# Optimization experiments

Measured on AMD Instinct MI355X. Metric: run time of the kernel, lower is better.

The kernel has to match this reference:

```python
import jax, jax.numpy as jnp
import numpy as np

K = 3          # number of nearest neighbors (pointops.interpolation uses k=3)
CHUNK = 4096   # fine-point chunk size for blocked kNN (bounds peak memory)
EPS = 1e-8     # inverse-distance epsilon, matches pointops interpolation


def _interpolate(xyz1, xyz2, feature2):
    """3-NN inverse-distance weighted interpolation from coarse (xyz2, feature2)
    onto fine points xyz1. Single batch (offsets cover all points)."""
    n1 = xyz1.shape[0]
    x2_sq = jnp.sum(xyz2 * xyz2, axis=-1)  # [N2]
    chunks = xyz1.reshape(n1 // CHUNK, CHUNK, 3)

    def body(q):  # q: [CHUNK, 3]
        q_sq = jnp.sum(q * q, axis=-1, keepdims=True)          # [CHUNK, 1]
        d2 = q_sq + x2_sq[None, :] - 2.0 * (q @ xyz2.T)        # [CHUNK, N2]
        neg_d2, idx = jax.lax.top_k(-d2, K)                    # 3 smallest
        dist = jnp.sqrt(jnp.maximum(-neg_d2, 1e-12))           # euclidean
        w = 1.0 / (dist + EPS)
        w = w / jnp.sum(w, axis=-1, keepdims=True)             # [CHUNK, K]
        return jnp.einsum('qk,qkc->qc', w, feature2[idx])      # [CHUNK, C]

    out = jax.lax.map(body, chunks)  # [n_chunks, CHUNK, C]
    return out.reshape(n1, -1)


def setup_inputs() -> dict:
    key = jax.random.key(0)
    k1, k2, k3, k4, k5, k6 = jax.random.split(key, 6)
    N1, N2, C, OUT = 32768, 8192, 256, 256
    xyz1 = jax.random.normal(k1, (N1, 3), dtype=jnp.float32)
    xyz2 = jax.random.normal(k2, (N2, 3), dtype=jnp.float32)
    feature1 = jax.random.normal(k3, (N1, C), dtype=jnp.float32)
    feature2 = jax.random.normal(k4, (N2, C), dtype=jnp.float32)
    offset1 = jnp.array([N1], dtype=jnp.int32)
    offset2 = jnp.array([N2], dtype=jnp.int32)
    W = jax.random.normal(k5, (OUT, C), dtype=jnp.float32) * (1.0 / np.sqrt(C))
    b = jax.random.normal(k6, (OUT,), dtype=jnp.float32) * 0.01
    return {"xyz1": xyz1, "xyz2": xyz2, "feature1": feature1,
            "feature2": feature2, "offset1": offset1, "offset2": offset2,
            "W": W, "b": b}


def reference(xyz1, xyz2, feature1, feature2, offset1, offset2, W, b):
    interp = _interpolate(xyz1, xyz2, feature2)  # [N1, C]
    return interp @ W.T + b                      # nn.Linear(in_coarse, out)
```

## Files before the change

kernel.cpp:

```cpp
#include <hip/hip_runtime.h>


#define FLT_BIG 3.402823466e+38f
#define CAP     16
#define MARGIN  3e-5f

__device__ __forceinline__ float rlf(float v, int l) {
    return __uint_as_float((unsigned)__builtin_amdgcn_readlane((int)__float_as_uint(v), l));
}

__global__ __launch_bounds__(256) void prep_kernel(const float* __restrict__ xyz2,
                                                   float4* __restrict__ pack, int N2) {
    int j = blockIdx.x * 256 + threadIdx.x;
    if (j < N2) {
        float x = xyz2[3 * j + 0];
        float y = xyz2[3 * j + 1];
        float z = xyz2[3 * j + 2];
        float4 p;
        p.x = x; p.y = y; p.z = z;
        p.w = 0.5f * (x * x + y * y + z * z);
        pack[j] = p;
    }
}

__global__ __launch_bounds__(256) void gemm_nt_f32(const float* __restrict__ A,
                                                   const float* __restrict__ B,
                                                   float* __restrict__ C,
                                                   int M, int N, int K) {
    __shared__ float As[64][68];
    __shared__ float Bs[64][68];

    const int t  = threadIdx.x;
    const int tx = t & 15;
    const int ty = t >> 4;
    const int bm = blockIdx.x * 64;
    const int bn = blockIdx.y * 64;

    float acc[4][4] = {{0.f}};

    for (int kt = 0; kt < K; kt += 64) {
#pragma unroll
        for (int rr = 0; rr < 4; ++rr) {
            int r = ty + 16 * rr;
            int c = tx * 4;
            float4 av = *(const float4*)(A + (size_t)(bm + r) * K + kt + c);
            As[c + 0][r] = av.x;
            As[c + 1][r] = av.y;
            As[c + 2][r] = av.z;
            As[c + 3][r] = av.w;
            float4 bv = *(const float4*)(B + (size_t)(bn + r) * K + kt + c);
            Bs[c + 0][r] = bv.x;
            Bs[c + 1][r] = bv.y;
            Bs[c + 2][r] = bv.z;
            Bs[c + 3][r] = bv.w;
        }
        __syncthreads();

#pragma unroll 8
        for (int k = 0; k < 64; ++k) {
            float4 a4 = *(const float4*)&As[k][ty * 4];
            float4 b4 = *(const float4*)&Bs[k][tx * 4];
            float a[4] = {a4.x, a4.y, a4.z, a4.w};
            float b[4] = {b4.x, b4.y, b4.z, b4.w};
#pragma unroll
            for (int i = 0; i < 4; ++i)
#pragma unroll
                for (int j = 0; j < 4; ++j)
                    acc[i][j] = fmaf(a[i], b[j], acc[i][j]);
        }
        __syncthreads();
    }

#pragma unroll
    for (int i = 0; i < 4; ++i) {
        float4 v;
        v.x = acc[i][0]; v.y = acc[i][1]; v.z = acc[i][2]; v.w = acc[i][3];
        *(float4*)(C + (size_t)(bm + ty * 4 + i) * N + bn + tx * 4) = v;
    }
}

#define TOP4V_INSERT(mv)                                           \
    do {                                                           \
        float _x  = (mv);                                          \
        float _n0 = fminf(b0, _x);  float _y0 = fmaxf(b0, _x); b0 = _n0; \
        float _n1 = fminf(b1, _y0); float _y1 = fmaxf(b1, _y0); b1 = _n1; \
        float _n2 = fminf(b2, _y1); float _y2 = fmaxf(b2, _y1); b2 = _n2; \
        b3 = fminf(b3, _y2);                                       \
    } while (0)

#define TOP3JD_INSERT(dd, j)                                       \
    do {                                                           \
        bool lt2 = ((dd) < d2v) || ((dd) == d2v && (j) < j2);      \
        if (lt2) {                                                 \
            bool lt1 = ((dd) < d1) || ((dd) == d1 && (j) < j1);    \
            if (lt1) {                                             \
                d2v = d1; j2 = j1;                                 \
                bool lt0 = ((dd) < d0) || ((dd) == d0 && (j) < j0);\
                if (lt0) { d1 = d0; j1 = j0; d0 = (dd); j0 = (j); }\
                else     { d1 = (dd); j1 = (j); }                  \
            } else { d2v = (dd); j2 = (j); }                       \
        }                                                          \
    } while (0)

#define DECLS(s) float px##s, py##s, pz##s, pw##s;
#define LOADS(s) { float4 _p = pack[base + ((s) << 6) + lane]; \
                   px##s = _p.x; py##s = _p.y; pz##s = _p.z; pw##s = _p.w; }
#define SAMPW(s) samp[wave][((s) << 6) + lane] = make_float4(px##s, py##s, pz##s, pw##s);
#define SLOTF(s)                                                               \
    {                                                                          \
        float acc = fmaf(qxx, px##s, fmaf(qyy, py##s, fmaf(qzz, pz##s, tq))); \
        unsigned long long mk = __ballot(acc >= pw##s);                        \
        while (mk) {                                                           \
            int l = __builtin_ctzll(mk);                                       \
            mk &= mk - 1;                                                      \
            if (is0 && cnt < CAP)                                              \
                myring[cnt] = (unsigned short)(base + ((s) << 6) + l);         \
            ++cnt;                                                             \
        }                                                                      \
    }
#define X16(M) M(0) M(1) M(2) M(3) M(4) M(5) M(6) M(7) \
               M(8) M(9) M(10) M(11) M(12) M(13) M(14) M(15)
#define X4(M)  M(0) M(1) M(2) M(3)

__global__ __launch_bounds__(512, 4) void knn_gather(const float* __restrict__ xyz1,
                                                     const float4* __restrict__ pack,
                                                     const float4* __restrict__ G4,
                                                     const float4* __restrict__ bias4,
                                                     float4* __restrict__ out4,
                                                     int N2) {
    __shared__ float4         samp[8][256];
    __shared__ float          mdl[64][25];
    __shared__ float          mdl4[64][33];
    __shared__ int            mil[64][25];
    __shared__ float          thr[64];
    __shared__ unsigned short ring[64][8 * CAP + 1];
    __shared__ unsigned short cnts[64][8];
    __shared__ float          swgt[64][3];
    __shared__ int            sidx[64][3];

    const int tid  = threadIdx.x;
    const int wave = __builtin_amdgcn_readfirstlane(tid >> 6);
    const int lane = tid & 63;
    const int fine = blockIdx.x * 64 + lane;

    const float qx = xyz1[3 * fine + 0];
    const float qy = xyz1[3 * fine + 1];
    const float qz = xyz1[3 * fine + 2];

    const int chunk = N2 >> 3;
    const int base  = wave * chunk;

    X16(DECLS)
    X16(LOADS)
    X4(SAMPW)
    __syncthreads();

    {
        float b0 = FLT_BIG, b1 = FLT_BIG, b2 = FLT_BIG, b3 = FLT_BIG;
        const float4* sp = samp[wave];
#pragma unroll 2
        for (int k = 0; k < 256; k += 4) {
            float4 p0 = sp[k + 0];
            float4 p1 = sp[k + 1];
            float4 p2 = sp[k + 2];
            float4 p3 = sp[k + 3];
            float m0 = p0.w - fmaf(qx, p0.x, fmaf(qy, p0.y, qz * p0.z));
            float m1 = p1.w - fmaf(qx, p1.x, fmaf(qy, p1.y, qz * p1.z));
            float m2 = p2.w - fmaf(qx, p2.x, fmaf(qy, p2.y, qz * p2.z));
            float m3 = p3.w - fmaf(qx, p3.x, fmaf(qy, p3.y, qz * p3.z));
            float mm = fminf(fminf(m0, m1), fminf(m2, m3));
            TOP4V_INSERT(mm);
        }
        mdl4[lane][wave * 4 + 0] = b0;
        mdl4[lane][wave * 4 + 1] = b1;
        mdl4[lane][wave * 4 + 2] = b2;
        mdl4[lane][wave * 4 + 3] = b3;
    }
    __syncthreads();

    if (tid < 64) {
        float b0 = FLT_BIG, b1 = FLT_BIG, b2 = FLT_BIG, b3 = FLT_BIG;
#pragma unroll
        for (int w = 0; w < 8; ++w)
#pragma unroll
            for (int k = 0; k < 4; ++k)
                TOP4V_INSERT(mdl4[tid][w * 4 + k]);
        thr[tid] = b3 + MARGIN;
    }
    __syncthreads();

    {
        const float qt_own = thr[lane];
        const bool  is0    = (lane == 0);
#pragma unroll 1
        for (int q = 0; q < 64; ++q) {
            float qxx = rlf(qx, q);
            float qyy = rlf(qy, q);
            float qzz = rlf(qz, q);
            float tq  = rlf(qt_own, q);
            int cnt = 0;
            unsigned short* myring = &ring[q][wave * CAP];
            X16(SLOTF)
            if (is0) cnts[q][wave] = (unsigned short)(cnt < CAP ? cnt : CAP);
        }
    }
    __syncthreads();

    {
        const int q  = tid >> 3;
        const int w  = tid & 7;
        const int fq = blockIdx.x * 64 + q;
        const float sqx = xyz1[3 * fq + 0];
        const float sqy = xyz1[3 * fq + 1];
        const float sqz = xyz1[3 * fq + 2];
        const float qsq = __fadd_rn(__fadd_rn(__fmul_rn(sqx, sqx), __fmul_rn(sqy, sqy)),
                                    __fmul_rn(sqz, sqz));
        float d0 = FLT_BIG, d1 = FLT_BIG, d2v = FLT_BIG;
        int   j0 = 0x7fffffff, j1 = 0x7fffffff, j2 = 0x7fffffff;
        const int n = (int)cnts[q][w];
        for (int e = 0; e < n; ++e) {
            const int j = ring[q][w * CAP + e];
            float4 p = pack[j];
            float x2s = __fadd_rn(__fadd_rn(__fmul_rn(p.x, p.x), __fmul_rn(p.y, p.y)),
                                  __fmul_rn(p.z, p.z));
            float dot = __fmaf_rn(sqz, p.z, __fmaf_rn(sqy, p.y, __fmul_rn(sqx, p.x)));
            float dd = __fsub_rn(__fadd_rn(qsq, x2s), __fmul_rn(2.0f, dot));
            TOP3JD_INSERT(dd, j);
        }
        mdl[q][w * 3 + 0] = d0;  mdl[q][w * 3 + 1] = d1;  mdl[q][w * 3 + 2] = d2v;
        mil[q][w * 3 + 0] = j0;  mil[q][w * 3 + 1] = j1;  mil[q][w * 3 + 2] = j2;
    }
    __syncthreads();

    if (tid < 64) {
        float d0 = FLT_BIG, d1 = FLT_BIG, d2v = FLT_BIG;
        int   j0 = 0x7fffffff, j1 = 0x7fffffff, j2 = 0x7fffffff;
#pragma unroll
        for (int w = 0; w < 8; ++w)
#pragma unroll
            for (int k = 0; k < 3; ++k) {
                float dd = mdl[tid][w * 3 + k];
                int   j  = mil[tid][w * 3 + k];
                TOP3JD_INSERT(dd, j);
            }
        float w0 = 1.0f / (__fadd_rn(sqrtf(fmaxf(d0,  1e-12f)), 1e-8f));
        float w1 = 1.0f / (__fadd_rn(sqrtf(fmaxf(d1,  1e-12f)), 1e-8f));
        float w2 = 1.0f / (__fadd_rn(sqrtf(fmaxf(d2v, 1e-12f)), 1e-8f));
        float wsum = __fadd_rn(__fadd_rn(w0, w1), w2);
        swgt[tid][0] = w0 / wsum; sidx[tid][0] = j0;
        swgt[tid][1] = w1 / wsum; sidx[tid][1] = j1;
        swgt[tid][2] = w2 / wsum; sidx[tid][2] = j2;
    }
    __syncthreads();

    const float4 bb = bias4[lane];
#pragma unroll
    for (int p = 0; p < 8; ++p) {
        int fl = wave * 8 + p;
        float w0 = swgt[fl][0];
        float w1 = swgt[fl][1];
        float w2 = swgt[fl][2];
        int j0 = sidx[fl][0];
        int j1 = sidx[fl][1];
        int j2 = sidx[fl][2];
        float4 g0 = G4[(size_t)j0 * 64 + lane];
        float4 g1 = G4[(size_t)j1 * 64 + lane];
        float4 g2 = G4[(size_t)j2 * 64 + lane];
        float4 o;
        o.x = fmaf(w0, g0.x, fmaf(w1, g1.x, fmaf(w2, g2.x, bb.x)));
        o.y = fmaf(w0, g0.y, fmaf(w1, g1.y, fmaf(w2, g2.y, bb.y)));
        o.z = fmaf(w0, g0.z, fmaf(w1, g1.z, fmaf(w2, g2.z, bb.z)));
        o.w = fmaf(w0, g0.w, fmaf(w1, g1.w, fmaf(w2, g2.w, bb.w)));
        out4[(size_t)(blockIdx.x * 64 + fl) * 64 + lane] = o;
    }
}

extern "C" void kernel_launch(void* const* d_in, const int* in_sizes, int n_in,
                              void* d_out, int out_size, void* d_ws, size_t ws_size,
                              hipStream_t stream) {
    const float* xyz1 = (const float*)d_in[0];
    const float* xyz2 = (const float*)d_in[1];
    const float* f2   = (const float*)d_in[3];
    const float* W    = (const float*)d_in[6];
    const float* bias = (const float*)d_in[7];

    const int N1  = in_sizes[0] / 3;
    const int N2  = in_sizes[1] / 3;
    const int C   = in_sizes[3] / N2;
    const int OUT = in_sizes[7];

    float*  G    = (float*)d_ws;
    float4* pack = (float4*)((char*)d_ws + (size_t)N2 * OUT * 4);

    prep_kernel<<<(N2 + 255) / 256, 256, 0, stream>>>(xyz2, pack, N2);

    dim3 ggrid(N2 / 64, OUT / 64);
    gemm_nt_f32<<<ggrid, 256, 0, stream>>>(f2, W, G, N2, OUT, C);

    knn_gather<<<N1 / 64, 512, 0, stream>>>(xyz1, pack, (const float4*)G,
                                            (const float4*)bias, (float4*)d_out, N2);
}
```

Before: 117.7 us.

## Use lane broadcasts instead of LDS samples and full candidate scan over all coarse points

Phase 1 drops the shared-memory sample buffer and its barrier: each wave keeps its 256 sample points in registers and broadcasts them with readlane. Phase 2 no longer holds only 1024 coarse points per wave. It now loops over four chunks of 256 points loaded from global memory, accumulating per-query counts through readlane/select. The point is to cut register pressure and LDS traffic so the occupancy hint in launch_bounds can be dropped. When the candidate ring overflows, the refinement step falls back to a brute-force scan of the wave's 1024 points for correctness. The cost is more scalar readlane work, a hardcoded 1024-point-per-wave split that assumes N2=8192, and a possibly expensive fallback path.

```diff
diff --git a/kernel.cpp b/kernel.cpp
--- a/kernel.cpp
+++ b/kernel.cpp
@@ -2,7 +2,8 @@
 
 
 #define FLT_BIG 3.402823466e+38f
-#define CAP     16
+#define CAP     14
+#define RROW    (8 * CAP + 1)
 #define MARGIN  3e-5f
 
 __device__ __forceinline__ float rlf(float v, int l) {
@@ -102,39 +103,53 @@
         }                                                          \
     } while (0)
 
-#define DECLS(s) float px##s, py##s, pz##s, pw##s;
-#define LOADS(s) { float4 _p = pack[base + ((s) << 6) + lane]; \
-                   px##s = _p.x; py##s = _p.y; pz##s = _p.z; pw##s = _p.w; }
-#define SAMPW(s) samp[wave][((s) << 6) + lane] = make_float4(px##s, py##s, pz##s, pw##s);
-#define SLOTF(s)                                                               \
+#define REF_D2(p)                                                              \
+    __fsub_rn(__fadd_rn(qsq, __fadd_rn(__fadd_rn(__fmul_rn((p).x, (p).x),      \
+                                                 __fmul_rn((p).y, (p).y)),     \
+                                       __fmul_rn((p).z, (p).z))),              \
+              __fmul_rn(2.0f, __fmaf_rn(sqz, (p).z,                            \
+                                __fmaf_rn(sqy, (p).y, __fmul_rn(sqx, (p).x)))))
+
+#define PH1_CHUNK(ch)                                                          \
+    for (int j = 0; j < 64; j += 4) {                                          \
+        float mm = FLT_BIG;                                                    \
+        _Pragma("unroll")                                                      \
+        for (int u = 0; u < 4; ++u) {                                          \
+            float sx = rlf(ch.x, j + u);                                       \
+            float sy = rlf(ch.y, j + u);                                       \
+            float sz = rlf(ch.z, j + u);                                       \
+            float sw = rlf(ch.w, j + u);                                       \
+            mm = fminf(mm, sw - fmaf(qx, sx, fmaf(qy, sy, qz * sz)));          \
+        }                                                                      \
+        TOP4V_INSERT(mm);                                                      \
+    }
+
+#define PH2_CHUNK(ch, cidx)                                                    \
     {                                                                          \
-        float acc = fmaf(qxx, px##s, fmaf(qyy, py##s, fmaf(qzz, pz##s, tq))); \
-        unsigned long long mk = __ballot(acc >= pw##s);                        \
+        float acc = fmaf(qxx, ch.x, fmaf(qyy, ch.y, fmaf(qzz, ch.z, tq)));     \
+        unsigned long long mk = __ballot(acc >= ch.w);                         \
         while (mk) {                                                           \
             int l = __builtin_ctzll(mk);                                       \
             mk &= mk - 1;                                                      \
-            if (is0 && cnt < CAP)                                              \
-                myring[cnt] = (unsigned short)(base + ((s) << 6) + l);         \
-            ++cnt;                                                             \
+            if (lane == 0 && cs < CAP)                                         \
+                ring[q][wave * CAP + cs] =                                     \
+                    (unsigned short)(obase + (cidx) * 64 + l);                 \
+            ++cs;                                                              \
         }                                                                      \
     }
-#define X16(M) M(0) M(1) M(2) M(3) M(4) M(5) M(6) M(7) \
-               M(8) M(9) M(10) M(11) M(12) M(13) M(14) M(15)
-#define X4(M)  M(0) M(1) M(2) M(3)
-
-__global__ __launch_bounds__(512, 4) void knn_gather(const float* __restrict__ xyz1,
-                                                     const float4* __restrict__ pack,
-                                                     const float4* __restrict__ G4,
-                                                     const float4* __restrict__ bias4,
-                                                     float4* __restrict__ out4,
-                                                     int N2) {
-    __shared__ float4         samp[8][256];
+
+__global__ __launch_bounds__(512) void knn_gather(const float* __restrict__ xyz1,
+                                                  const float4* __restrict__ pack,
+                                                  const float4* __restrict__ G4,
+                                                  const float4* __restrict__ bias4,
+                                                  float4* __restrict__ out4,
+                                                  int N2) {
+    __shared__ float          mdl4[64][33];
+    __shared__ float          thr[64];
+    __shared__ unsigned short ring[64][RROW];
+    __shared__ unsigned char  cnts[64][8];
     __shared__ float          mdl[64][25];
-    __shared__ float          mdl4[64][33];
     __shared__ int            mil[64][25];
-    __shared__ float          thr[64];
-    __shared__ unsigned short ring[64][8 * CAP + 1];
-    __shared__ unsigned short cnts[64][8];
     __shared__ float          swgt[64][3];
     __shared__ int            sidx[64][3];
 
@@ -147,30 +162,18 @@
     const float qy = xyz1[3 * fine + 1];
     const float qz = xyz1[3 * fine + 2];
 
-    const int chunk = N2 >> 3;
-    const int base  = wave * chunk;
-
-    X16(DECLS)
-    X16(LOADS)
-    X4(SAMPW)
-    __syncthreads();
+    const int wbase = wave * 1024;
 
     {
+        float4 s0 = pack[wbase +   0 + lane];
+        float4 s1 = pack[wbase +  64 + lane];
+        float4 s2 = pack[wbase + 128 + lane];
+        float4 s3 = pack[wbase + 192 + lane];
         float b0 = FLT_BIG, b1 = FLT_BIG, b2 = FLT_BIG, b3 = FLT_BIG;
-        const float4* sp = samp[wave];
-#pragma unroll 2
-        for (int k = 0; k < 256; k += 4) {
-            float4 p0 = sp[k + 0];
-            float4 p1 = sp[k + 1];
-            float4 p2 = sp[k + 2];
-            float4 p3 = sp[k + 3];
-            float m0 = p0.w - fmaf(qx, p0.x, fmaf(qy, p0.y, qz * p0.z));
-            float m1 = p1.w - fmaf(qx, p1.x, fmaf(qy, p1.y, qz * p1.z));
-            float m2 = p2.w - fmaf(qx, p2.x, fmaf(qy, p2.y, qz * p2.z));
-            float m3 = p3.w - fmaf(qx, p3.x, fmaf(qy, p3.y, qz * p3.z));
-            float mm = fminf(fminf(m0, m1), fminf(m2, m3));
-            TOP4V_INSERT(mm);
-        }
+        PH1_CHUNK(s0)
+        PH1_CHUNK(s1)
+        PH1_CHUNK(s2)
+        PH1_CHUNK(s3)
         mdl4[lane][wave * 4 + 0] = b0;
         mdl4[lane][wave * 4 + 1] = b1;
         mdl4[lane][wave * 4 + 2] = b2;
@@ -190,19 +193,30 @@
     __syncthreads();
 
     {
-        const float qt_own = thr[lane];
-        const bool  is0    = (lane == 0);
+        const float tv = thr[lane];
+        int cntv = 0;
 #pragma unroll 1
-        for (int q = 0; q < 64; ++q) {
-            float qxx = rlf(qx, q);
-            float qyy = rlf(qy, q);
-            float qzz = rlf(qz, q);
-            float tq  = rlf(qt_own, q);
-            int cnt = 0;
-            unsigned short* myring = &ring[q][wave * CAP];
-            X16(SLOTF)
-            if (is0) cnts[q][wave] = (unsigned short)(cnt < CAP ? cnt : CAP);
+        for (int o = 0; o < 4; ++o) {
+            const int obase = wbase + o * 256;
+            float4 c0 = pack[obase +   0 + lane];
+            float4 c1 = pack[obase +  64 + lane];
+            float4 c2 = pack[obase + 128 + lane];
+            float4 c3 = pack[obase + 192 + lane];
+#pragma unroll 1
+            for (int q = 0; q < 64; ++q) {
+                float qxx = rlf(qx, q);
+                float qyy = rlf(qy, q);
+                float qzz = rlf(qz, q);
+                float tq  = rlf(tv, q);
+                int cs = __builtin_amdgcn_readlane(cntv, q);
+                PH2_CHUNK(c0, 0)
+                PH2_CHUNK(c1, 1)
+                PH2_CHUNK(c2, 2)
+                PH2_CHUNK(c3, 3)
+                cntv = (lane == q) ? cs : cntv;
+            }
         }
+        cnts[lane][wave] = (unsigned char)min(cntv, 255);
     }
     __syncthreads();
 
@@ -217,15 +231,23 @@
                                     __fmul_rn(sqz, sqz));
         float d0 = FLT_BIG, d1 = FLT_BIG, d2v = FLT_BIG;
         int   j0 = 0x7fffffff, j1 = 0x7fffffff, j2 = 0x7fffffff;
-        const int n = (int)cnts[q][w];
-        for (int e = 0; e < n; ++e) {
-            const int j = ring[q][w * CAP + e];
-            float4 p = pack[j];
-            float x2s = __fadd_rn(__fadd_rn(__fmul_rn(p.x, p.x), __fmul_rn(p.y, p.y)),
-                                  __fmul_rn(p.z, p.z));
-            float dot = __fmaf_rn(sqz, p.z, __fmaf_rn(sqy, p.y, __fmul_rn(sqx, p.x)));
-            float dd = __fsub_rn(__fadd_rn(qsq, x2s), __fmul_rn(2.0f, dot));
-            TOP3JD_INSERT(dd, j);
+        const int rawn = (int)cnts[q][w];
+        if (rawn <= CAP) {
+#pragma unroll 1
+            for (int e = 0; e < rawn; ++e) {
+                const int j = ring[q][w * CAP + e];
+                float4 p = pack[j];
+                float dd = REF_D2(p);
+                TOP3JD_INSERT(dd, j);
+            }
+        } else {
+            const int gb = w * 1024;
+#pragma unroll 1
+            for (int j = gb; j < gb + 1024; ++j) {
+                float4 p = pack[j];
+                float dd = REF_D2(p);
+                TOP3JD_INSERT(dd, j);
+            }
         }
         mdl[q][w * 3 + 0] = d0;  mdl[q][w * 3 + 1] = d1;  mdl[q][w * 3 + 2] = d2v;
         mil[q][w * 3 + 0] = j0;  mil[q][w * 3 + 1] = j1;  mil[q][w * 3 + 2] = j2;
```

Measured after the change: 159.3 us. 1.35x slower.
